# Optimization experiments

Measured on AMD Instinct MI355X. Metric: run time of the kernel, lower is better.

The kernel has to match this reference:

```python
import jax, jax.numpy as jnp
import numpy as np

# static graph/layer sizes
N_SRC0, N_DST0 = 60000, 15000
N_DST1 = 4000
H1, D1 = 8, 256   # layer1: 8 heads, 256 per head
H2, D2 = 1, 128   # layer2: 1 head, 128 (= out_feats)
IN_DIM = H1 * D1  # 2048


def gat_conv(feat, W, al, ar, b, src, dst, n_dst, H, D, act):
    # feat: [N_src, F]; W: [F, H*D]; al/ar: [H, D]; b: [H*D]
    h = (feat @ W).reshape(feat.shape[0], H, D)          # [N_src, H, D]
    el = jnp.einsum('nhd,hd->nh', h, al)                 # [N_src, H]
    er = jnp.einsum('nhd,hd->nh', h[:n_dst], ar)         # [N_dst, H]
    e = jax.nn.leaky_relu(el[src] + er[dst], 0.2)        # [E, H]
    # edge softmax grouped by destination node (numerically stable)
    emax = jax.ops.segment_max(e, dst, num_segments=n_dst)
    emax = jnp.where(jnp.isfinite(emax), emax, 0.0)      # guard zero-in-degree dsts
    ex = jnp.exp(e - emax[dst])
    denom = jax.ops.segment_sum(ex, dst, num_segments=n_dst)
    a = ex / denom[dst]                                  # [E, H]
    out = jax.ops.segment_sum(h[src] * a[:, :, None], dst, num_segments=n_dst)
    out = out + b.reshape(1, H, D)
    return jax.nn.relu(out) if act else out              # [N_dst, H, D]


def setup_inputs() -> dict:
    key = jax.random.key(0)
    ks = jax.random.split(key, 16)
    feat = jax.random.normal(ks[0], (N_SRC0, IN_DIM), dtype=jnp.float32)
    src0 = jax.random.randint(ks[1], (240000,), 0, N_SRC0, dtype=jnp.int32)
    dst0 = jax.random.randint(ks[2], (240000,), 0, N_DST0, dtype=jnp.int32)
    src1 = jax.random.randint(ks[3], (64000,), 0, N_DST0, dtype=jnp.int32)
    dst1 = jax.random.randint(ks[4], (64000,), 0, N_DST1, dtype=jnp.int32)
    # layer1 params (in 2048 -> 8 heads x 256)
    W1 = jax.random.normal(ks[5], (IN_DIM, H1 * D1), dtype=jnp.float32) / np.sqrt(IN_DIM)
    al1 = jax.random.normal(ks[6], (H1, D1), dtype=jnp.float32) / np.sqrt(D1)
    ar1 = jax.random.normal(ks[7], (H1, D1), dtype=jnp.float32) / np.sqrt(D1)
    b1 = jnp.zeros((H1 * D1,), dtype=jnp.float32)
    # layer2 params (in 256 (post head-mean) -> 1 head x 128)
    W2 = jax.random.normal(ks[8], (D1, H2 * D2), dtype=jnp.float32) / np.sqrt(D1)
    al2 = jax.random.normal(ks[9], (H2, D2), dtype=jnp.float32) / np.sqrt(D2)
    ar2 = jax.random.normal(ks[10], (H2, D2), dtype=jnp.float32) / np.sqrt(D2)
    b2 = jnp.zeros((H2 * D2,), dtype=jnp.float32)
    return {"feat": feat, "W1": W1, "al1": al1, "ar1": ar1, "b1": b1,
            "W2": W2, "al2": al2, "ar2": ar2, "b2": b2,
            "src0": src0, "dst0": dst0, "src1": src1, "dst1": dst1}


def reference(feat, W1, al1, ar1, b1, W2, al2, ar2, b2, src0, dst0, src1, dst1):
    h = gat_conv(feat, W1, al1, ar1, b1, src0, dst0, N_DST0, H1, D1, act=True)
    h = h.mean(axis=1)                                   # head mean -> [N_DST0, 256]
    h = gat_conv(h, W2, al2, ar2, b2, src1, dst1, N_DST1, H2, D2, act=False)
    return h.reshape(N_DST1, H2 * D2)                    # flatten(1) -> [4000, 128]
```

## Files before the change

kernel.cpp:

```cpp
#include <hip/hip_runtime.h>
#include <hip/hip_bf16.h>


typedef __bf16 bf16;
typedef bf16 bf16x8 __attribute__((ext_vector_type(8)));
typedef float f32x4 __attribute__((ext_vector_type(4)));

#define N_SRC0V 60000
#define N_DST0V 15000
#define N_DST1V 4000
#define E0V 240000
#define E1V 64000
#define HD1V 2048
#define K1V 2048
#define M1PAD 60160
#define M2PAD 15104

#define BM 128
#define BN 128
#define BK 64

#define GBM 256
#define GBN 256
#define GBK 32

__device__ __forceinline__ void gload16(const void* g, void* l) {
  __builtin_amdgcn_global_load_lds(
      (__attribute__((address_space(1))) void*)(g),
      (__attribute__((address_space(3))) void*)(l), 16, 0, 0);
}

__global__ void k_convert(const float* __restrict__ x, bf16* __restrict__ y, long n8) {
  long i = (long)blockIdx.x * 256 + threadIdx.x;
  if (i >= n8) return;
  const float4* xp = (const float4*)(x + i * 8);
  float4 a = xp[0], b = xp[1];
  bf16x8 o;
  o[0] = (bf16)a.x; o[1] = (bf16)a.y; o[2] = (bf16)a.z; o[3] = (bf16)a.w;
  o[4] = (bf16)b.x; o[5] = (bf16)b.y; o[6] = (bf16)b.z; o[7] = (bf16)b.w;
  *(bf16x8*)(y + i * 8) = o;
}

__global__ void k_transpose_bf16(const float* __restrict__ W, bf16* __restrict__ WT,
                                 int R, int C) {
  __shared__ float tile[32][33];
  int tx = threadIdx.x & 31, ty = threadIdx.x >> 5;
  int c0 = blockIdx.x * 32, r0 = blockIdx.y * 32;
  for (int i = ty; i < 32; i += 8) {
    int r = r0 + i, c = c0 + tx;
    tile[i][tx] = (r < R && c < C) ? W[(size_t)r * C + c] : 0.f;
  }
  __syncthreads();
  for (int i = ty; i < 32; i += 8) {
    int c = c0 + i, r = r0 + tx;
    if (c < C && r < R) WT[(size_t)c * R + r] = (bf16)tile[tx][i];
  }
}

__global__ __launch_bounds__(512, 2) void k_gemm256_bt(
    const bf16* __restrict__ A, const bf16* __restrict__ BT,
    bf16* __restrict__ C, int N, int K) {
  extern __shared__ char smem_raw[];
  bf16* smem = (bf16*)smem_raw;
  const int tid = threadIdx.x;
  const int lane = tid & 63;
  const int wv = tid >> 6;
  const int wm = wv >> 2;
  const int wn = wv & 3;
  const int lr = lane & 15, lq = lane >> 4;

  int nwg = gridDim.x * gridDim.y;
  int flat = blockIdx.y * gridDim.x + blockIdx.x;
  if ((nwg & 7) == 0) {
    int cpx = nwg >> 3;
    flat = (flat & 7) * cpx + (flat >> 3);
  }
  const int m0 = (flat / gridDim.x) * GBM;
  const int n0 = (flat % gridDim.x) * GBN;

  const f32x4 vzero = {0.f, 0.f, 0.f, 0.f};
  f32x4 acc[8][4];
#pragma unroll
  for (int i = 0; i < 8; ++i)
#pragma unroll
    for (int j = 0; j < 4; ++j) acc[i][j] = vzero;

  auto stage = [&](int b, int k0) {
    bf16* sAb = smem + b * 16384;
    bf16* sBb = sAb + 8192;
#pragma unroll
    for (int it = 0; it < 2; ++it) {
      int c = it * 512 + tid;
      int ln = c & 63;
      int row = (c >> 6) * 16 + (ln & 15);
      int col = (ln >> 4) * 8;
      gload16(A + (size_t)(m0 + row) * K + k0 + col, &sAb[c * 8]);
    }
#pragma unroll
    for (int it = 0; it < 2; ++it) {
      int c = it * 512 + tid;
      int ln = c & 63;
      int row = (c >> 6) * 16 + (ln & 15);
      int col = (ln >> 4) * 8;
      gload16(BT + (size_t)(n0 + row) * K + k0 + col, &sBb[c * 8]);
    }
  };

  const int NT = K / GBK;
  stage(0, 0);
  stage(1, GBK);
  stage(2, 2 * GBK);

  for (int kt = 0; kt < NT; ++kt) {
    const int cb = kt & 3;
    const bf16* sAb = smem + cb * 16384;
    const bf16* sBb = sAb + 8192;

    if (kt < NT - 2) {
      asm volatile("s_waitcnt vmcnt(8)" ::: "memory");
    } else if (kt == NT - 2) {
      asm volatile("s_waitcnt vmcnt(4)" ::: "memory");
    } else {
      asm volatile("s_waitcnt vmcnt(0)" ::: "memory");
    }
    __builtin_amdgcn_sched_barrier(0);
    __builtin_amdgcn_s_barrier();
    __builtin_amdgcn_sched_barrier(0);

    if (kt + 3 < NT) stage((kt + 3) & 3, (kt + 3) * GBK);

    bf16x8 af[8], bfr[4];
#pragma unroll
    for (int j = 0; j < 4; ++j)
      bfr[j] = *(const bf16x8*)&sBb[((wn * 4 + j) * 64 + lane) * 8];
#pragma unroll
    for (int i = 0; i < 8; ++i)
      af[i] = *(const bf16x8*)&sAb[((wm * 8 + i) * 64 + lane) * 8];
    __builtin_amdgcn_sched_barrier(0);
    asm volatile("s_waitcnt lgkmcnt(0)" ::: "memory");
    __builtin_amdgcn_sched_barrier(0);
    __builtin_amdgcn_s_setprio(1);
#pragma unroll
    for (int i = 0; i < 8; ++i)
#pragma unroll
      for (int j = 0; j < 4; ++j)
        acc[i][j] = __builtin_amdgcn_mfma_f32_16x16x32_bf16(af[i], bfr[j], acc[i][j], 0, 0, 0);
    __builtin_amdgcn_s_setprio(0);
    __builtin_amdgcn_sched_barrier(0);
  }

#pragma unroll
  for (int i = 0; i < 8; ++i)
#pragma unroll
    for (int j = 0; j < 4; ++j) {
      int row = m0 + wm * 128 + i * 16 + lq * 4;
      int col = n0 + wn * 64 + j * 16 + lr;
#pragma unroll
      for (int r = 0; r < 4; ++r)
        C[(size_t)(row + r) * N + col] = (bf16)acc[i][j][r];
    }
}

template <typename OutT>
__global__ __launch_bounds__(256) void k_gemm_bt(
    const bf16* __restrict__ A, const bf16* __restrict__ BT,
    OutT* __restrict__ C, int N, int K) {
  __shared__ bf16 sA[BM * BK];
  __shared__ bf16 sB[BN * BK];
  const int tid = threadIdx.x;
  const int lane = tid & 63;
  const int wv = tid >> 6;
  const int wm = wv >> 1, wn = wv & 1;
  const int lr = lane & 15, lq = lane >> 4;
  const int m0 = blockIdx.y * BM;
  const int n0 = blockIdx.x * BN;

  const f32x4 vzero = {0.f, 0.f, 0.f, 0.f};
  f32x4 acc[4][4];
#pragma unroll
  for (int i = 0; i < 4; ++i)
#pragma unroll
    for (int j = 0; j < 4; ++j) acc[i][j] = vzero;

  for (int k0 = 0; k0 < K; k0 += BK) {
#pragma unroll
    for (int it = 0; it < 4; ++it) {
      int c = it * 256 + tid;
      int seg = c >> 6;
      int ln = c & 63;
      int row = (seg >> 1) * 16 + (ln & 15);
      int col = (seg & 1) * 32 + (ln >> 4) * 8;
      gload16(A + (size_t)(m0 + row) * K + k0 + col, &sA[c * 8]);
      gload16(BT + (size_t)(n0 + row) * K + k0 + col, &sB[c * 8]);
    }
    __syncthreads();
#pragma unroll
    for (int kk = 0; kk < BK; kk += 32) {
      const int kb = kk >> 5;
      bf16x8 af[4], bfr[4];
#pragma unroll
      for (int i = 0; i < 4; ++i)
        af[i] = *(const bf16x8*)&sA[(((wm * 4 + i) * 2 + kb) * 64 + lane) * 8];
#pragma unroll
      for (int j = 0; j < 4; ++j)
        bfr[j] = *(const bf16x8*)&sB[(((wn * 4 + j) * 2 + kb) * 64 + lane) * 8];
#pragma unroll
      for (int i = 0; i < 4; ++i)
#pragma unroll
        for (int j = 0; j < 4; ++j)
          acc[i][j] = __builtin_amdgcn_mfma_f32_16x16x32_bf16(af[i], bfr[j], acc[i][j], 0, 0, 0);
    }
    __syncthreads();
  }
#pragma unroll
  for (int i = 0; i < 4; ++i)
#pragma unroll
    for (int j = 0; j < 4; ++j) {
      int row = m0 + wm * 64 + i * 16 + lq * 4;
      int col = n0 + wn * 64 + j * 16 + lr;
#pragma unroll
      for (int r = 0; r < 4; ++r)
        C[(size_t)(row + r) * N + col] = (OutT)acc[i][j][r];
    }
}

__global__ void k_el_er1(const bf16* __restrict__ h, const float* __restrict__ al,
                         const float* __restrict__ ar, float* __restrict__ el,
                         float* __restrict__ er, int n_dst) {
  int row = blockIdx.x;
  int t = threadIdx.x;
  bf16x8 hv = *(const bf16x8*)(h + (size_t)row * 2048 + t * 8);
  float pl = 0.f, pr = 0.f;
#pragma unroll
  for (int e = 0; e < 8; ++e) {
    float v = (float)hv[e];
    pl += v * al[t * 8 + e];
    pr += v * ar[t * 8 + e];
  }
#pragma unroll
  for (int off = 16; off >= 1; off >>= 1) {
    pl += __shfl_down(pl, off);
    pr += __shfl_down(pr, off);
  }
  if ((t & 31) == 0) {
    el[(size_t)row * 8 + (t >> 5)] = pl;
    if (row < n_dst) er[(size_t)row * 8 + (t >> 5)] = pr;
  }
}

__global__ void k_el_er2(const float* __restrict__ h, const float* __restrict__ al,
                         const float* __restrict__ ar, float* __restrict__ el,
                         float* __restrict__ er, int n_el, int n_dst) {
  int t = threadIdx.x;
  int row = blockIdx.x * 16 + (t >> 4);
  int s = t & 15;
  const float* hp = h + (size_t)row * 128 + s * 8;
  float4 a = *(const float4*)hp;
  float4 b = *(const float4*)(hp + 4);
  float pl = a.x * al[s * 8] + a.y * al[s * 8 + 1] + a.z * al[s * 8 + 2] + a.w * al[s * 8 + 3]
           + b.x * al[s * 8 + 4] + b.y * al[s * 8 + 5] + b.z * al[s * 8 + 6] + b.w * al[s * 8 + 7];
  float pr = a.x * ar[s * 8] + a.y * ar[s * 8 + 1] + a.z * ar[s * 8 + 2] + a.w * ar[s * 8 + 3]
           + b.x * ar[s * 8 + 4] + b.y * ar[s * 8 + 5] + b.z * ar[s * 8 + 6] + b.w * ar[s * 8 + 7];
#pragma unroll
  for (int off = 8; off >= 1; off >>= 1) {
    pl += __shfl_down(pl, off);
    pr += __shfl_down(pr, off);
  }
  if (s == 0 && row < n_el) {
    el[row] = pl;
    if (row < n_dst) er[row] = pr;
  }
}

__global__ void k_zero(int* __restrict__ p, int n) {
  int i = blockIdx.x * 256 + threadIdx.x;
  if (i < n) p[i] = 0;
}
__global__ void k_hist(const int* __restrict__ d, int E, int* __restrict__ counts) {
  int e = blockIdx.x * 256 + threadIdx.x;
  if (e < E) atomicAdd(&counts[d[e]], 1);
}
__global__ void k_scan(const int* __restrict__ counts, int n, int* __restrict__ offs,
                       int* __restrict__ cursor) {
  __shared__ int part[1024];
  int t = threadIdx.x;
  int per = (n + 1023) >> 10;
  int b = t * per;
  int e = b + per < n ? b + per : n;
  int s = 0;
  for (int i = b; i < e; ++i) s += counts[i];
  part[t] = s;
  __syncthreads();
  for (int off = 1; off < 1024; off <<= 1) {
    int v = 0;
    if (t >= off) v = part[t - off];
    __syncthreads();
    part[t] += v;
    __syncthreads();
  }
  int run = (t == 0) ? 0 : part[t - 1];
  for (int i = b; i < e; ++i) { offs[i] = run; cursor[i] = run; run += counts[i]; }
  if (t == 1023) offs[n] = run;
}
__global__ void k_scatter(const int* __restrict__ d, int E, int* __restrict__ cursor,
                          int* __restrict__ eperm) {
  int e = blockIdx.x * 256 + threadIdx.x;
  if (e < E) eperm[atomicAdd(&cursor[d[e]], 1)] = e;
}

__global__ void k_stats(const int* __restrict__ offs, const int* __restrict__ eperm,
                        const int* __restrict__ srcv, const float* __restrict__ el,
                        const float* __restrict__ er, int n_dst, int H,
                        float* __restrict__ emax, float* __restrict__ eden) {
  int idx = blockIdx.x * 256 + threadIdx.x;
  if (idx >= n_dst * H) return;
  int dn = idx / H, hh = idx - dn * H;
  int s0 = offs[dn], s1 = offs[dn + 1];
  float erv = er[idx];
  float mx = -1e30f;
  for (int p = s0; p < s1; ++p) {
    float v = el[srcv[eperm[p]] * H + hh] + erv;
    v = v > 0.f ? v : 0.2f * v;
    mx = fmaxf(mx, v);
  }
  if (s1 == s0) mx = 0.f;
  float s = 0.f;
  for (int p = s0; p < s1; ++p) {
    float v = el[srcv[eperm[p]] * H + hh] + erv;
    v = v > 0.f ? v : 0.2f * v;
    s += expf(v - mx);
  }
  emax[idx] = mx;
  eden[idx] = s;
}

__global__ __launch_bounds__(256) void k_aggr1(
    const int* __restrict__ offs, const int* __restrict__ eperm,
    const int* __restrict__ srcv, const float* __restrict__ el,
    const float* __restrict__ er, const float* __restrict__ emax,
    const float* __restrict__ eden, const bf16* __restrict__ h1,
    const float* __restrict__ b1, bf16* __restrict__ outm) {
  int dn = blockIdx.x;
  int t = threadIdx.x;
  int head = t >> 5;
  int jd = (t & 31) << 3;
  __shared__ float wbuf[32][8];
  __shared__ int sidx[32];
  __shared__ float obuf[2048];
  float acc[8] = {0.f, 0.f, 0.f, 0.f, 0.f, 0.f, 0.f, 0.f};
  int s0 = offs[dn], s1 = offs[dn + 1];
  for (int base = s0; base < s1; base += 32) {
    int rem = s1 - base;
    int cnt = rem < 32 ? rem : 32;
    __syncthreads();
    if (t < cnt * 8) {
      int ec = t >> 3, hh = t & 7;
      int e = eperm[base + ec];
      int sv = srcv[e];
      if (hh == 0) sidx[ec] = sv;
      float v = el[sv * 8 + hh] + er[dn * 8 + hh];
      v = v > 0.f ? v : 0.2f * v;
      float den = eden[dn * 8 + hh];
      wbuf[ec][hh] = den > 0.f ? expf(v - emax[dn * 8 + hh]) / den : 0.f;
    }
    __syncthreads();
    for (int ec = 0; ec < cnt; ++ec) {
      float w = wbuf[ec][head];
      const bf16* hp = h1 + (size_t)sidx[ec] * 2048 + (head << 8) + jd;
      bf16x8 x = *(const bf16x8*)hp;
#pragma unroll
      for (int e2 = 0; e2 < 8; ++e2) acc[e2] += w * (float)x[e2];
    }
  }
  int ob = (head << 8) + jd;
#pragma unroll
  for (int k2 = 0; k2 < 8; ++k2) {
    float v = acc[k2] + b1[ob + k2];
    obuf[ob + k2] = v > 0.f ? v : 0.f;
  }
  __syncthreads();
  float sum = 0.f;
#pragma unroll
  for (int hh = 0; hh < 8; ++hh) sum += obuf[hh * 256 + t];
  outm[(size_t)dn * 256 + t] = (bf16)(sum * 0.125f);
}

__global__ __launch_bounds__(128) void k_aggr2(
    const int* __restrict__ offs, const int* __restrict__ eperm,
    const int* __restrict__ srcv, const float* __restrict__ el,
    const float* __restrict__ er, const float* __restrict__ emax,
    const float* __restrict__ eden, const float* __restrict__ h2,
    const float* __restrict__ b2, float* __restrict__ out) {
  int dn = blockIdx.x;
  int t = threadIdx.x;
  __shared__ float wbuf[64];
  __shared__ int sidx[64];
  float acc = 0.f;
  int s0 = offs[dn], s1 = offs[dn + 1];
  float erv = er[dn], mx = emax[dn], den = eden[dn];
  for (int base = s0; base < s1; base += 64) {
    int rem = s1 - base;
    int cnt = rem < 64 ? rem : 64;
    __syncthreads();
    if (t < cnt) {
      int e = eperm[base + t];
      int sv = srcv[e];
      sidx[t] = sv;
      float v = el[sv] + erv;
      v = v > 0.f ? v : 0.2f * v;
      wbuf[t] = den > 0.f ? expf(v - mx) / den : 0.f;
    }
    __syncthreads();
    for (int ec = 0; ec < cnt; ++ec)
      acc += wbuf[ec] * h2[(size_t)sidx[ec] * 128 + t];
  }
  out[(size_t)dn * 128 + t] = acc + b2[t];
}

extern "C" void kernel_launch(void* const* d_in, const int* in_sizes, int n_in,
                              void* d_out, int out_size, void* d_ws, size_t ws_size,
                              hipStream_t stream) {
  const float* feat = (const float*)d_in[0];
  const float* W1   = (const float*)d_in[1];
  const float* al1  = (const float*)d_in[2];
  const float* ar1  = (const float*)d_in[3];
  const float* b1   = (const float*)d_in[4];
  const float* W2   = (const float*)d_in[5];
  const float* al2  = (const float*)d_in[6];
  const float* ar2  = (const float*)d_in[7];
  const float* b2   = (const float*)d_in[8];
  const int* src0   = (const int*)d_in[9];
  const int* dst0   = (const int*)d_in[10];
  const int* src1   = (const int*)d_in[11];
  const int* dst1   = (const int*)d_in[12];
  float* out = (float*)d_out;

  static bool s_attr_set = false;
  if (!s_attr_set) {
    hipFuncSetAttribute(reinterpret_cast<const void*>(k_gemm256_bt),
                        hipFuncAttributeMaxDynamicSharedMemorySize, 131072);
    s_attr_set = true;
  }

  char* w = (char*)d_ws;
  auto alloc = [&](size_t bytes) {
    char* p = w;
    w += (bytes + 255) & ~(size_t)255;
    return p;
  };
  bf16*  featb   = (bf16*)alloc((size_t)M1PAD * K1V * 2);
  bf16*  w1t     = (bf16*)alloc((size_t)HD1V * K1V * 2);
  bf16*  w2t     = (bf16*)alloc((size_t)128 * 256 * 2);
  bf16*  h1      = (bf16*)alloc((size_t)M1PAD * HD1V * 2);
  float* el1     = (float*)alloc((size_t)N_SRC0V * 8 * 4);
  float* er1     = (float*)alloc((size_t)N_DST0V * 8 * 4);
  float* emax1   = (float*)alloc((size_t)N_DST0V * 8 * 4);
  float* eden1   = (float*)alloc((size_t)N_DST0V * 8 * 4);
  bf16*  outm    = (bf16*)alloc((size_t)M2PAD * 256 * 2);
  float* h2      = (float*)alloc((size_t)M2PAD * 128 * 4);
  float* el2     = (float*)alloc((size_t)N_DST0V * 4);
  float* er2     = (float*)alloc((size_t)N_DST1V * 4);
  float* emax2   = (float*)alloc((size_t)N_DST1V * 4);
  float* eden2   = (float*)alloc((size_t)N_DST1V * 4);
  int*   counts1 = (int*)alloc((size_t)N_DST0V * 4);
  int*   offs1   = (int*)alloc((size_t)(N_DST0V + 1) * 4);
  int*   cursor1 = (int*)alloc((size_t)N_DST0V * 4);
  int*   eperm1  = (int*)alloc((size_t)E0V * 4);
  int*   counts2 = (int*)alloc((size_t)N_DST1V * 4);
  int*   offs2   = (int*)alloc((size_t)(N_DST1V + 1) * 4);
  int*   cursor2 = (int*)alloc((size_t)N_DST1V * 4);
  int*   eperm2  = (int*)alloc((size_t)E1V * 4);

  k_zero<<<(N_DST0V + 255) / 256, 256, 0, stream>>>(counts1, N_DST0V);
  k_zero<<<(N_DST1V + 255) / 256, 256, 0, stream>>>(counts2, N_DST1V);
  {
    long n8 = (long)N_SRC0V * K1V / 8;
    k_convert<<<(unsigned)((n8 + 255) / 256), 256, 0, stream>>>(feat, featb, n8);
    int padi = (M1PAD - N_SRC0V) * K1V / 2;
    k_zero<<<(padi + 255) / 256, 256, 0, stream>>>(
        (int*)(featb + (size_t)N_SRC0V * K1V), padi);
  }
  k_transpose_bf16<<<dim3(64, 64), 256, 0, stream>>>(W1, w1t, K1V, HD1V);
  k_transpose_bf16<<<dim3(4, 8), 256, 0, stream>>>(W2, w2t, 256, 128);

  k_gemm256_bt<<<dim3(HD1V / GBN, M1PAD / GBM), 512, 131072, stream>>>(
      featb, w1t, h1, HD1V, K1V);
  k_el_er1<<<N_SRC0V, 256, 0, stream>>>(h1, al1, ar1, el1, er1, N_DST0V);
  k_hist<<<(E0V + 255) / 256, 256, 0, stream>>>(dst0, E0V, counts1);
  k_scan<<<1, 1024, 0, stream>>>(counts1, N_DST0V, offs1, cursor1);
  k_scatter<<<(E0V + 255) / 256, 256, 0, stream>>>(dst0, E0V, cursor1, eperm1);
  k_stats<<<(N_DST0V * 8 + 255) / 256, 256, 0, stream>>>(offs1, eperm1, src0, el1, er1,
                                                         N_DST0V, 8, emax1, eden1);
  k_aggr1<<<N_DST0V, 256, 0, stream>>>(offs1, eperm1, src0, el1, er1, emax1, eden1,
                                       h1, b1, outm);

  k_gemm_bt<float><<<dim3(1, M2PAD / BM), 256, 0, stream>>>(outm, w2t, h2, 128, 256);
  k_el_er2<<<M2PAD / 16, 256, 0, stream>>>(h2, al2, ar2, el2, er2, N_DST0V, N_DST1V);
  k_hist<<<(E1V + 255) / 256, 256, 0, stream>>>(dst1, E1V, counts2);
  k_scan<<<1, 1024, 0, stream>>>(counts2, N_DST1V, offs2, cursor2);
  k_scatter<<<(E1V + 255) / 256, 256, 0, stream>>>(dst1, E1V, cursor2, eperm2);
  k_stats<<<(N_DST1V + 255) / 256, 256, 0, stream>>>(offs2, eperm2, src1, el2, er2,
                                                     N_DST1V, 1, emax2, eden2);
  k_aggr2<<<N_DST1V, 128, 0, stream>>>(offs2, eperm2, src1, el2, er2, emax2, eden2,
                                       h2, b2, out);
}
```

Baseline: 1.604 ms.

## Double-buffer LDS fragment registers to overlap loads with MFMA in big GEMM

Restructures the GEMM main loop to unroll by two and keep two register sets of A/B fragments. The next tile's LDS fragment reads are issued before the current tile's MFMAs, so the explicit lgkmcnt(0) wait ahead of the compute is removed. This aims to hide LDS read latency behind matrix work. In exchange it raises VGPR pressure, which could lower occupancy, and the vmcnt/barrier accounting becomes harder to verify.

```diff
diff --git a/kernel.cpp b/kernel.cpp
--- a/kernel.cpp
+++ b/kernel.cpp
@@ -106,47 +106,58 @@
     }
   };
 
+  auto ldfrag = [&](int b, bf16x8* af, bf16x8* bf) {
+    const bf16* sAb = smem + b * 16384;
+    const bf16* sBb = sAb + 8192;
+#pragma unroll
+    for (int j = 0; j < 4; ++j)
+      bf[j] = *(const bf16x8*)&sBb[((wn * 4 + j) * 64 + lane) * 8];
+#pragma unroll
+    for (int i = 0; i < 8; ++i)
+      af[i] = *(const bf16x8*)&sAb[((wm * 8 + i) * 64 + lane) * 8];
+  };
+
   const int NT = K / GBK;
   stage(0, 0);
   stage(1, GBK);
   stage(2, 2 * GBK);
 
-  for (int kt = 0; kt < NT; ++kt) {
-    const int cb = kt & 3;
-    const bf16* sAb = smem + cb * 16384;
-    const bf16* sBb = sAb + 8192;
-
-    if (kt < NT - 2) {
-      asm volatile("s_waitcnt vmcnt(8)" ::: "memory");
-    } else if (kt == NT - 2) {
-      asm volatile("s_waitcnt vmcnt(4)" ::: "memory");
-    } else {
-      asm volatile("s_waitcnt vmcnt(0)" ::: "memory");
-    }
-    __builtin_amdgcn_sched_barrier(0);
+  asm volatile("s_waitcnt vmcnt(8)" ::: "memory");
+  __builtin_amdgcn_s_barrier();
+  __builtin_amdgcn_sched_barrier(0);
+
+  bf16x8 afA[8], bfA[4], afB[8], bfB[4];
+  ldfrag(0, afA, bfA);
+
+  for (int kt = 0; kt < NT; kt += 2) {
+    if (kt + 2 < NT) asm volatile("s_waitcnt vmcnt(4)" ::: "memory");
+    else             asm volatile("s_waitcnt vmcnt(0)" ::: "memory");
     __builtin_amdgcn_s_barrier();
     __builtin_amdgcn_sched_barrier(0);
-
+    ldfrag((kt + 1) & 3, afB, bfB);
     if (kt + 3 < NT) stage((kt + 3) & 3, (kt + 3) * GBK);
-
-    bf16x8 af[8], bfr[4];
-#pragma unroll
-    for (int j = 0; j < 4; ++j)
-      bfr[j] = *(const bf16x8*)&sBb[((wn * 4 + j) * 64 + lane) * 8];
+    __builtin_amdgcn_s_setprio(1);
 #pragma unroll
     for (int i = 0; i < 8; ++i)
-      af[i] = *(const bf16x8*)&sAb[((wm * 8 + i) * 64 + lane) * 8];
-    __builtin_amdgcn_sched_barrier(0);
-    asm volatile("s_waitcnt lgkmcnt(0)" ::: "memory");
-    __builtin_amdgcn_sched_barrier(0);
+#pragma unroll
+      for (int j = 0; j < 4; ++j)
+        acc[i][j] = __builtin_amdgcn_mfma_f32_16x16x32_bf16(afA[i], bfA[j], acc[i][j], 0, 0, 0);
+    __builtin_amdgcn_s_setprio(0);
+
+    if (kt + 2 < NT) {
+      asm volatile("s_waitcnt vmcnt(4)" ::: "memory");
+      __builtin_amdgcn_s_barrier();
+      __builtin_amdgcn_sched_barrier(0);
+      ldfrag((kt + 2) & 3, afA, bfA);
+      if (kt + 4 < NT) stage((kt + 4) & 3, (kt + 4) * GBK);
+    }
     __builtin_amdgcn_s_setprio(1);
 #pragma unroll
     for (int i = 0; i < 8; ++i)
 #pragma unroll
       for (int j = 0; j < 4; ++j)
-        acc[i][j] = __builtin_amdgcn_mfma_f32_16x16x32_bf16(af[i], bfr[j], acc[i][j], 0, 0, 0);
+        acc[i][j] = __builtin_amdgcn_mfma_f32_16x16x32_bf16(afB[i], bfB[j], acc[i][j], 0, 0, 0);
     __builtin_amdgcn_s_setprio(0);
-    __builtin_amdgcn_sched_barrier(0);
   }
 
 #pragma unroll
```

After: 1.604 ms. Within noise of the previous version (-0.0%).
